# Performance work log

Hardware: AMD Instinct MI355X
Metric: run time of the kernel (lower is better)

## Reference

```python
import jax, jax.numpy as jnp
import numpy as np

STRIDE = 2
CAPS_DIM = 8  # out_channels: capsule dimensionality
EPS = 1e-8


def _squash(s):
    # Canonical capsule squash along the last (capsule-dim) axis:
    # v = (||s||^2 / (1 + ||s||^2)) * s / ||s||
    sq_norm = jnp.sum(s * s, axis=-1, keepdims=True)  # [B, N, 1]
    scale = sq_norm / (1.0 + sq_norm) / jnp.sqrt(sq_norm + EPS)
    return scale * s


def setup_inputs() -> dict:
    key = jax.random.key(0)
    kx, kw = jax.random.split(key)
    x = jax.random.normal(kx, (64, 256, 40, 40), dtype=jnp.float32)
    W = jax.random.normal(kw, (256, 256, 9, 9), dtype=jnp.float32) * 0.02
    b = jnp.zeros((256,), dtype=jnp.float32)
    return {"x": x, "W": W, "b": b}


def reference(x, W, b):
    # Conv2d: NCHW input, OIHW kernel, stride 2, VALID padding -> (64,256,16,16)
    out = jax.lax.conv_general_dilated(
        x, W,
        window_strides=(STRIDE, STRIDE),
        padding="VALID",
        dimension_numbers=("NCHW", "OIHW", "NCHW"),
    ) + b[None, :, None, None]
    batch_size = out.shape[0]
    caps = out.reshape(batch_size, -1, CAPS_DIM)  # (64, 8192, 8)
    return _squash(caps)
```

## Files before the change

### kernel.cpp

```cpp
#include <hip/hip_runtime.h>


typedef __attribute__((ext_vector_type(8))) short bf16x8;
typedef __attribute__((ext_vector_type(4))) float f32x4;

static __device__ __forceinline__ unsigned short f2bf(float f) {
  unsigned u = __builtin_bit_cast(unsigned, f);
  u += 0x7FFFu + ((u >> 16) & 1u);
  return (unsigned short)(u >> 16);
}

static __device__ __forceinline__ void gll16(const void* g, void* l) {
  typedef __attribute__((address_space(1))) const unsigned char AS1;
  typedef __attribute__((address_space(3))) unsigned char AS3;
  __builtin_amdgcn_global_load_lds((AS1*)g, (AS3*)l, 16, 0, 0);
}

__global__ __launch_bounds__(256) void prep_w_k(const float* __restrict__ W,
                                                unsigned short* __restrict__ Wb) {
  __shared__ float t[5184];
  int bid = blockIdx.x;
  int oc = bid >> 2, ict = bid & 3;
  const float* src = W + ((size_t)oc * 256 + (size_t)ict * 64) * 81;
  for (int i = threadIdx.x; i < 5184; i += 256) t[i] = src[i];
  __syncthreads();
  unsigned short* dst = Wb + (size_t)oc * 20736 + ict * 64;
  for (int i = threadIdx.x; i < 5184; i += 256) {
    int khw = i >> 6, ic = i & 63;
    dst[(size_t)khw * 256 + ic] = f2bf(t[ic * 81 + khw]);
  }
}

__global__ __launch_bounds__(256) void prep_x_k(const float* __restrict__ x,
                                                unsigned short* __restrict__ Xt) {
  __shared__ float t[64][41];
  int bid = blockIdx.x;
  int ict = bid & 3;
  int ih = (bid >> 2) % 40;
  int b  = bid / 160;
  const float* src = x + (((size_t)(b * 256 + ict * 64) * 40) + ih) * 40;
  for (int i = threadIdx.x; i < 2560; i += 256) {
    int ic = i / 40, iw = i - ic * 40;
    t[ic][iw] = src[(size_t)ic * 1600 + iw];
  }
  __syncthreads();
  unsigned short* dst = Xt + ((size_t)(b * 40 + ih) * 40) * 256 + ict * 64;
  for (int i = threadIdx.x; i < 1280; i += 256) {
    int iw = i >> 5, icp = i & 31;
    unsigned lo = f2bf(t[icp * 2][iw]);
    unsigned hi = f2bf(t[icp * 2 + 1][iw]);
    *(unsigned*)(dst + (size_t)iw * 256 + icp * 2) = (hi << 16) | lo;
  }
}

__global__ __launch_bounds__(256) void gemm_k(const unsigned short* __restrict__ Wb,
                                              const unsigned short* __restrict__ Xt,
                                              float* __restrict__ Cp, int kts) {
  __shared__ __align__(16) short Asm[8192];
  __shared__ __align__(16) short Bsm[8192];
  const int tid = threadIdx.x;
  const int l = tid & 63, w = tid >> 6;
  const int wm = w >> 1, wn = w & 1;
  const int nc = blockIdx.x, mr = blockIdx.y, sz = blockIdx.z;
  const int b = nc >> 1, ohb = (nc & 1) << 3;
  const int ocb = mr << 7;

  const int lrow  = l >> 3;
  const int lslot = l & 7;
  const int chunk = ((lslot ^ lrow) << 3);

  unsigned aoff[4], boff[4];
#pragma unroll
  for (int i = 0; i < 4; ++i) {
    int rloc = ((w * 4 + i) << 3) + lrow;
    aoff[i] = (unsigned)(ocb + rloc) * 20736u + (unsigned)chunk;
    int ohl = rloc >> 4, owl = rloc & 15;
    boff[i] = (unsigned)(((b * 40 + 2 * (ohb + ohl)) * 40) + 2 * owl) * 256u + (unsigned)chunk;
  }

  const int fr = l & 15;
  const int kq = l >> 4;
  int arow[4], brow[4];
#pragma unroll
  for (int i = 0; i < 4; ++i) {
    arow[i] = wm * 64 + i * 16 + fr;
    brow[i] = wn * 64 + i * 16 + fr;
  }

  f32x4 acc[4][4];
#pragma unroll
  for (int mi = 0; mi < 4; ++mi)
#pragma unroll
    for (int ni = 0; ni < 4; ++ni) acc[mi][ni] = (f32x4){0.f, 0.f, 0.f, 0.f};

  const int kt0 = sz * kts, kt1 = kt0 + kts;
  for (int kt = kt0; kt < kt1; ++kt) {
    const int khw = kt >> 2, ict = kt & 3;
    const int kh = khw / 9, kw = khw - kh * 9;
    const unsigned ka = (unsigned)kt << 6;
    const unsigned kb = (unsigned)((kh * 40 + kw) << 8) + (unsigned)(ict << 6);
#pragma unroll
    for (int i = 0; i < 4; ++i) {
      gll16(Wb + aoff[i] + ka, Asm + ((w * 4 + i) << 9));
      gll16(Xt + boff[i] + kb, Bsm + ((w * 4 + i) << 9));
    }
    __syncthreads();
#pragma unroll
    for (int kk = 0; kk < 2; ++kk) {
      const int kc = (kk << 2) + kq;
      bf16x8 af[4], bg[4];
#pragma unroll
      for (int i = 0; i < 4; ++i) {
        af[i] = *(const bf16x8*)(Asm + (arow[i] << 6) + ((kc ^ (arow[i] & 7)) << 3));
        bg[i] = *(const bf16x8*)(Bsm + (brow[i] << 6) + ((kc ^ (brow[i] & 7)) << 3));
      }
#pragma unroll
      for (int mi = 0; mi < 4; ++mi)
#pragma unroll
        for (int ni = 0; ni < 4; ++ni)
          acc[mi][ni] = __builtin_amdgcn_mfma_f32_16x16x32_bf16(af[mi], bg[ni], acc[mi][ni], 0, 0, 0);
    }
    __syncthreads();
  }

  float* Co = Cp + (size_t)sz * 4194304;
  const int nbase = nc << 7;
#pragma unroll
  for (int mi = 0; mi < 4; ++mi) {
#pragma unroll
    for (int ni = 0; ni < 4; ++ni) {
      int ocr = ocb + wm * 64 + mi * 16 + kq * 4;
      int n = nbase + wn * 64 + ni * 16 + fr;
#pragma unroll
      for (int r = 0; r < 4; ++r)
        Co[(size_t)(ocr + r) * 16384 + n] = acc[mi][ni][r];
    }
  }
}

__global__ __launch_bounds__(256) void finish_k(const float* __restrict__ Cp,
                                                const float* __restrict__ bias,
                                                float* __restrict__ out, int S) {
  int cap = blockIdx.x * 256 + threadIdx.x;
  int b = cap >> 13;
  int flat = (cap & 8191) << 3;
  int oc = flat >> 8;
  size_t cbase = (size_t)oc * 16384 + (size_t)b * 256 + (size_t)(flat & 255);
  float v[8];
#pragma unroll
  for (int i = 0; i < 8; ++i) v[i] = 0.f;
  for (int s = 0; s < S; ++s) {
    const float4* p = (const float4*)(Cp + (size_t)s * 4194304 + cbase);
    float4 a0 = p[0], a1 = p[1];
    v[0] += a0.x; v[1] += a0.y; v[2] += a0.z; v[3] += a0.w;
    v[4] += a1.x; v[5] += a1.y; v[6] += a1.z; v[7] += a1.w;
  }
  float bb = bias[oc];
  float sq = 0.f;
#pragma unroll
  for (int i = 0; i < 8; ++i) { v[i] += bb; sq += v[i] * v[i]; }
  float scale = sq / ((1.0f + sq) * sqrtf(sq + 1e-8f));
  float4 o0 = make_float4(v[0] * scale, v[1] * scale, v[2] * scale, v[3] * scale);
  float4 o1 = make_float4(v[4] * scale, v[5] * scale, v[6] * scale, v[7] * scale);
  float4* q = (float4*)(out + (size_t)cap * 8);
  q[0] = o0; q[1] = o1;
}

extern "C" void kernel_launch(void* const* d_in, const int* in_sizes, int n_in,
                              void* d_out, int out_size, void* d_ws, size_t ws_size,
                              hipStream_t stream) {
  const float* x    = (const float*)d_in[0];
  const float* W    = (const float*)d_in[1];
  const float* bias = (const float*)d_in[2];
  float* out = (float*)d_out;
  char* ws = (char*)d_ws;

  unsigned short* Xt = (unsigned short*)ws;
  unsigned short* Wb = (unsigned short*)(ws + 52428800ull);
  float*          Cp = (float*)(ws + 63045632ull);

  const size_t slice = 16777216ull;
  int S = 1;
  if (ws_size >= 63045632ull + 4 * slice) S = 4;
  else if (ws_size >= 63045632ull + 2 * slice) S = 2;

  prep_x_k<<<10240, 256, 0, stream>>>(x, Xt);
  prep_w_k<<<1024, 256, 0, stream>>>(W, Wb);
  gemm_k<<<dim3(128, 2, S), 256, 0, stream>>>(Wb, Xt, Cp, 324 / S);
  finish_k<<<2048, 256, 0, stream>>>(Cp, bias, out, S);
}
```

Measured before the change: 412.1 us.

## Double-buffer GEMM with 256x256 tiles, 512 threads, and merged prep kernels

Restructures the conv GEMM so each 512-thread block computes a full 256-oc by 256-pixel tile (one image per block), using a double-buffered LDS pipeline. Next-tile loads are issued before computing the current one, with explicit vmcnt waits, raw barriers and setprio around the MFMA bursts. The two prep kernels are merged into one launch, and x is loaded with float4. Each block gets more data reuse and hides load latency, but the grid shrinks to 64*S blocks with 128 KB of LDS each, which may hurt occupancy and CU coverage.

```diff
diff --git a/kernel.cpp b/kernel.cpp
--- a/kernel.cpp
+++ b/kernel.cpp
@@ -3,6 +3,10 @@
 
 typedef __attribute__((ext_vector_type(8))) short bf16x8;
 typedef __attribute__((ext_vector_type(4))) float f32x4;
+
+#define SBAR __builtin_amdgcn_sched_barrier(0)
+#define HBAR __builtin_amdgcn_s_barrier()
+#define CFEN asm volatile("" ::: "memory")
 
 static __device__ __forceinline__ unsigned short f2bf(float f) {
   unsigned u = __builtin_bit_cast(unsigned, f);
@@ -16,124 +20,168 @@
   __builtin_amdgcn_global_load_lds((AS1*)g, (AS3*)l, 16, 0, 0);
 }
 
-__global__ __launch_bounds__(256) void prep_w_k(const float* __restrict__ W,
-                                                unsigned short* __restrict__ Wb) {
+__global__ __launch_bounds__(256) void prep_k(const float* __restrict__ x,
+                                              const float* __restrict__ W,
+                                              unsigned short* __restrict__ Xt,
+                                              unsigned short* __restrict__ Wb) {
   __shared__ float t[5184];
-  int bid = blockIdx.x;
-  int oc = bid >> 2, ict = bid & 3;
-  const float* src = W + ((size_t)oc * 256 + (size_t)ict * 64) * 81;
-  for (int i = threadIdx.x; i < 5184; i += 256) t[i] = src[i];
-  __syncthreads();
-  unsigned short* dst = Wb + (size_t)oc * 20736 + ict * 64;
-  for (int i = threadIdx.x; i < 5184; i += 256) {
-    int khw = i >> 6, ic = i & 63;
-    dst[(size_t)khw * 256 + ic] = f2bf(t[ic * 81 + khw]);
-  }
-}
-
-__global__ __launch_bounds__(256) void prep_x_k(const float* __restrict__ x,
-                                                unsigned short* __restrict__ Xt) {
-  __shared__ float t[64][41];
-  int bid = blockIdx.x;
-  int ict = bid & 3;
-  int ih = (bid >> 2) % 40;
-  int b  = bid / 160;
-  const float* src = x + (((size_t)(b * 256 + ict * 64) * 40) + ih) * 40;
-  for (int i = threadIdx.x; i < 2560; i += 256) {
-    int ic = i / 40, iw = i - ic * 40;
-    t[ic][iw] = src[(size_t)ic * 1600 + iw];
-  }
-  __syncthreads();
-  unsigned short* dst = Xt + ((size_t)(b * 40 + ih) * 40) * 256 + ict * 64;
-  for (int i = threadIdx.x; i < 1280; i += 256) {
-    int iw = i >> 5, icp = i & 31;
-    unsigned lo = f2bf(t[icp * 2][iw]);
-    unsigned hi = f2bf(t[icp * 2 + 1][iw]);
-    *(unsigned*)(dst + (size_t)iw * 256 + icp * 2) = (hi << 16) | lo;
-  }
-}
-
-__global__ __launch_bounds__(256) void gemm_k(const unsigned short* __restrict__ Wb,
-                                              const unsigned short* __restrict__ Xt,
-                                              float* __restrict__ Cp, int kts) {
-  __shared__ __align__(16) short Asm[8192];
-  __shared__ __align__(16) short Bsm[8192];
+  int bx = blockIdx.x;
+  if (bx < 10240) {
+    int ict = bx & 3;
+    int ih = (bx >> 2) % 40;
+    int b  = bx / 160;
+    const float4* src4 = (const float4*)(x + ((size_t)(b * 256 + ict * 64) * 40 + ih) * 40);
+    for (int i = threadIdx.x; i < 640; i += 256) {
+      int ic = i / 10, q = i - ic * 10;
+      float4 v = src4[ic * 400 + q];
+      float* tr = t + ic * 41 + q * 4;
+      tr[0] = v.x; tr[1] = v.y; tr[2] = v.z; tr[3] = v.w;
+    }
+    __syncthreads();
+    unsigned short* dst = Xt + ((size_t)(b * 40 + ih) * 40) * 256 + ict * 64;
+    for (int i = threadIdx.x; i < 1280; i += 256) {
+      int iw = i >> 5, icp = i & 31;
+      unsigned lo = f2bf(t[(icp * 2) * 41 + iw]);
+      unsigned hi = f2bf(t[(icp * 2 + 1) * 41 + iw]);
+      *(unsigned*)(dst + (size_t)iw * 256 + icp * 2) = (hi << 16) | lo;
+    }
+  } else {
+    int bid = bx - 10240;
+    int oc = bid >> 2, ict = bid & 3;
+    const float* src = W + ((size_t)oc * 256 + (size_t)ict * 64) * 81;
+    for (int i = threadIdx.x; i < 5184; i += 256) t[i] = src[i];
+    __syncthreads();
+    unsigned short* dst = Wb + (size_t)oc * 20736 + ict * 64;
+    for (int i = threadIdx.x; i < 5184; i += 256) {
+      int khw = i >> 6, ic = i & 63;
+      dst[(size_t)khw * 256 + ic] = f2bf(t[ic * 81 + khw]);
+    }
+  }
+}
+
+__global__ __launch_bounds__(512, 2) void gemm_k(const unsigned short* __restrict__ Wb,
+                                                 const unsigned short* __restrict__ Xt,
+                                                 float* __restrict__ Cp, int kts) {
+  __shared__ __align__(16) short LDS[65536];
   const int tid = threadIdx.x;
   const int l = tid & 63, w = tid >> 6;
-  const int wm = w >> 1, wn = w & 1;
-  const int nc = blockIdx.x, mr = blockIdx.y, sz = blockIdx.z;
-  const int b = nc >> 1, ohb = (nc & 1) << 3;
-  const int ocb = mr << 7;
-
-  const int lrow  = l >> 3;
-  const int lslot = l & 7;
-  const int chunk = ((lslot ^ lrow) << 3);
-
-  unsigned aoff[4], boff[4];
-#pragma unroll
-  for (int i = 0; i < 4; ++i) {
-    int rloc = ((w * 4 + i) << 3) + lrow;
-    aoff[i] = (unsigned)(ocb + rloc) * 20736u + (unsigned)chunk;
-    int ohl = rloc >> 4, owl = rloc & 15;
-    boff[i] = (unsigned)(((b * 40 + 2 * (ohb + ohl)) * 40) + 2 * owl) * 256u + (unsigned)chunk;
-  }
-
-  const int fr = l & 15;
-  const int kq = l >> 4;
-  int arow[4], brow[4];
-#pragma unroll
-  for (int i = 0; i < 4; ++i) {
-    arow[i] = wm * 64 + i * 16 + fr;
-    brow[i] = wn * 64 + i * 16 + fr;
-  }
-
-  f32x4 acc[4][4];
-#pragma unroll
-  for (int mi = 0; mi < 4; ++mi)
+  const int wm = w >> 2, wn = w & 3;
+  const int nc = blockIdx.x, sz = blockIdx.z;
+
+  const int lrow = l >> 3, lslot = l & 7;
+  const int chunk = (lslot ^ lrow) << 3;
+
+  unsigned aoffA[2], boffB[2];
+  int dstA[2], dstB[2];
+#pragma unroll
+  for (int h = 0; h < 2; ++h) {
+    int srow = h * 128 + w * 16 + lrow;
+    aoffA[h] = (unsigned)srow * 20736u + (unsigned)chunk;
+    int oh = h * 8 + w, ow = lrow;
+    boffB[h] = (unsigned)((nc * 40 + 2 * oh) * 40 + 2 * ow) * 256u + (unsigned)chunk;
+    dstA[h] = (h * 128 + w * 16) << 6;
+    dstB[h] = 32768 + dstA[h];
+  }
+
+  const int fr = l & 15, kq = l >> 4, sw = fr & 7;
+  const int arow0 = wm * 128 + fr;
+  const int brow0 = wn * 64 + fr;
+
+  f32x4 acc[8][4];
+#pragma unroll
+  for (int mi = 0; mi < 8; ++mi)
 #pragma unroll
     for (int ni = 0; ni < 4; ++ni) acc[mi][ni] = (f32x4){0.f, 0.f, 0.f, 0.f};
 
-  const int kt0 = sz * kts, kt1 = kt0 + kts;
-  for (int kt = kt0; kt < kt1; ++kt) {
-    const int khw = kt >> 2, ict = kt & 3;
-    const int kh = khw / 9, kw = khw - kh * 9;
-    const unsigned ka = (unsigned)kt << 6;
-    const unsigned kb = (unsigned)((kh * 40 + kw) << 8) + (unsigned)(ict << 6);
-#pragma unroll
-    for (int i = 0; i < 4; ++i) {
-      gll16(Wb + aoff[i] + ka, Asm + ((w * 4 + i) << 9));
-      gll16(Xt + boff[i] + kb, Bsm + ((w * 4 + i) << 9));
-    }
-    __syncthreads();
-#pragma unroll
-    for (int kk = 0; kk < 2; ++kk) {
-      const int kc = (kk << 2) + kq;
-      bf16x8 af[4], bg[4];
-#pragma unroll
-      for (int i = 0; i < 4; ++i) {
-        af[i] = *(const bf16x8*)(Asm + (arow[i] << 6) + ((kc ^ (arow[i] & 7)) << 3));
-        bg[i] = *(const bf16x8*)(Bsm + (brow[i] << 6) + ((kc ^ (brow[i] & 7)) << 3));
+  const int kt0 = sz * kts, nkt = kts;
+
+  {
+    const unsigned ka0 = (unsigned)kt0 << 6;
+    const int khw0 = kt0 >> 2, ict0 = kt0 & 3;
+    const int kh0 = khw0 / 9, kw0 = khw0 - kh0 * 9;
+    const unsigned kb0 = (unsigned)((kh0 * 40 + kw0) << 8) + (unsigned)(ict0 << 6);
+#pragma unroll
+    for (int h = 0; h < 2; ++h) {
+      gll16(Wb + aoffA[h] + ka0, LDS + dstA[h]);
+      gll16(Wb + aoffA[h] + ka0 + 8u * 20736u, LDS + dstA[h] + 512);
+      gll16(Xt + boffB[h] + kb0, LDS + dstB[h]);
+      gll16(Xt + boffB[h] + kb0 + 4096u, LDS + dstB[h] + 512);
+    }
+  }
+
+#define DO_PHASE(P)                                                              \
+  {                                                                              \
+    bf16x8 af[2][2];                                                             \
+    _Pragma("unroll") for (int j = 0; j < 2; ++j)                                \
+    _Pragma("unroll") for (int kk = 0; kk < 2; ++kk) {                           \
+      int row = arow0 + (2 * (P) + j) * 16;                                      \
+      int kc = kk * 4 + kq;                                                      \
+      af[j][kk] = *(const bf16x8*)(LDS + buf + (row << 6) + ((kc ^ sw) << 3));   \
+    }                                                                            \
+    __builtin_amdgcn_s_setprio(1);                                               \
+    _Pragma("unroll") for (int j = 0; j < 2; ++j)                                \
+    _Pragma("unroll") for (int ni = 0; ni < 4; ++ni)                             \
+    _Pragma("unroll") for (int kk = 0; kk < 2; ++kk)                             \
+      acc[2 * (P) + j][ni] = __builtin_amdgcn_mfma_f32_16x16x32_bf16(            \
+          af[j][kk], bg[ni][kk], acc[2 * (P) + j][ni], 0, 0, 0);                 \
+    __builtin_amdgcn_s_setprio(0);                                               \
+  }
+
+  for (int t = 0; t < nkt; ++t) {
+    const int kt = kt0 + t;
+    const int buf = (t & 1) << 14;
+    const int nb = buf ^ 16384;
+    const unsigned kaN = (unsigned)(kt + 1) << 6;
+    const int ktn = kt + 1;
+    const int khwN = ktn >> 2, ictN = ktn & 3;
+    const int khN = khwN / 9, kwN = khwN - khN * 9;
+    const unsigned kbN = (unsigned)((khN * 40 + kwN) << 8) + (unsigned)(ictN << 6);
+    const bool more = (t + 1 < nkt);
+
+    SBAR; HBAR; CFEN;
+    if (more) {
+#pragma unroll
+      for (int h = 0; h < 2; ++h) {
+        gll16(Wb + aoffA[h] + kaN, LDS + nb + dstA[h]);
+        gll16(Wb + aoffA[h] + kaN + 8u * 20736u, LDS + nb + dstA[h] + 512);
+        gll16(Xt + boffB[h] + kbN, LDS + nb + dstB[h]);
+        gll16(Xt + boffB[h] + kbN + 4096u, LDS + nb + dstB[h] + 512);
       }
-#pragma unroll
-      for (int mi = 0; mi < 4; ++mi)
-#pragma unroll
-        for (int ni = 0; ni < 4; ++ni)
-          acc[mi][ni] = __builtin_amdgcn_mfma_f32_16x16x32_bf16(af[mi], bg[ni], acc[mi][ni], 0, 0, 0);
-    }
-    __syncthreads();
-  }
+      SBAR;
+      asm volatile("s_waitcnt vmcnt(8)" ::: "memory");
+    } else {
+      SBAR;
+      asm volatile("s_waitcnt vmcnt(0)" ::: "memory");
+    }
+    HBAR; CFEN; SBAR;
+
+    bf16x8 bg[4][2];
+#pragma unroll
+    for (int ni = 0; ni < 4; ++ni)
+#pragma unroll
+      for (int kk = 0; kk < 2; ++kk) {
+        int row = brow0 + ni * 16;
+        int kc = kk * 4 + kq;
+        bg[ni][kk] = *(const bf16x8*)(LDS + 32768 + buf + (row << 6) + ((kc ^ sw) << 3));
+      }
+
+    DO_PHASE(0)
+    DO_PHASE(1)
+    DO_PHASE(2)
+    DO_PHASE(3)
+  }
+#undef DO_PHASE
 
   float* Co = Cp + (size_t)sz * 4194304;
-  const int nbase = nc << 7;
-#pragma unroll
-  for (int mi = 0; mi < 4; ++mi) {
+#pragma unroll
+  for (int mi = 0; mi < 8; ++mi) {
 #pragma unroll
     for (int ni = 0; ni < 4; ++ni) {
-      int ocr = ocb + wm * 64 + mi * 16 + kq * 4;
-      int n = nbase + wn * 64 + ni * 16 + fr;
+      int oc = wm * 128 + mi * 16 + kq * 4;
+      int n = (nc << 8) + wn * 64 + ni * 16 + fr;
 #pragma unroll
       for (int r = 0; r < 4; ++r)
-        Co[(size_t)(ocr + r) * 16384 + n] = acc[mi][ni][r];
+        Co[(size_t)(oc + r) * 16384 + n] = acc[mi][ni][r];
     }
   }
 }
@@ -184,8 +232,7 @@
   if (ws_size >= 63045632ull + 4 * slice) S = 4;
   else if (ws_size >= 63045632ull + 2 * slice) S = 2;
 
-  prep_x_k<<<10240, 256, 0, stream>>>(x, Xt);
-  prep_w_k<<<1024, 256, 0, stream>>>(W, Wb);
-  gemm_k<<<dim3(128, 2, S), 256, 0, stream>>>(Wb, Xt, Cp, 324 / S);
+  prep_k<<<11264, 256, 0, stream>>>(x, W, Xt, Wb);
+  gemm_k<<<dim3(64, 1, S), 512, 0, stream>>>(Wb, Xt, Cp, 324 / S);
   finish_k<<<2048, 256, 0, stream>>>(Cp, bias, out, S);
 }
```

Measured after the change: 341.1 us. -17.2%, faster.
